# Optimization experiments

Measured on AMD Instinct MI355X. Metric: run time of the kernel, lower is better.

The kernel has to match this reference:

```python
import jax, jax.numpy as jnp
import numpy as np
from jax import lax

B, C, H, WIN, K = 8, 128, 128, 4, 3
WS = H // 2           # window_size = input_resolution / sqrt(win_num)
L = H * H
DN = ('NCHW', 'OIHW', 'NCHW')


def setup_inputs() -> dict:
    key = jax.random.key(0)
    ks = jax.random.split(key, 12)
    s = 0.02
    return {
        'x': jax.random.normal(ks[0], (B, L, C), jnp.float32),
        # ConvLayer1 params: (win_num*dim, dim, k, k), grouped conv, no bias
        'conv1_w': jax.random.normal(ks[1], (WIN * C, C, K, K), jnp.float32) * s,
        'dc_w': jax.random.normal(ks[2], (WIN, C), jnp.float32) * s,
        'dc_b': jax.random.normal(ks[3], (WIN,), jnp.float32) * s,
        'l1_w': jax.random.normal(ks[4], (4 * WIN, WIN), jnp.float32) * s,
        'l1_b': jax.random.normal(ks[5], (4 * WIN,), jnp.float32) * s,
        'l2_w': jax.random.normal(ks[6], (WIN, 4 * WIN), jnp.float32) * s,
        'l2_b': jax.random.normal(ks[7], (WIN,), jnp.float32) * s,
        'gk_w': jax.random.normal(ks[8], (C, WIN, C), jnp.float32) * s,
        'gk_b': jax.random.normal(ks[9], (C,), jnp.float32) * s,
        'fusion_w': jax.random.normal(ks[10], (C, (WIN + 1) * C), jnp.float32) * s,
        'fusion_b': jax.random.normal(ks[11], (C,), jnp.float32) * s,
    }


def reference(x, conv1_w, dc_w, dc_b, l1_w, l1_b, l2_w, l2_b, gk_w, gk_b, fusion_w, fusion_b):
    Bx = x.shape[0]
    # ka_window_partition: (B, L, C) -> (B, win_num*C, WS, WS), window-major channels
    xw = x.reshape(Bx, 2, WS, 2, WS, C).transpose(0, 1, 3, 5, 2, 4).reshape(Bx, WIN * C, WS, WS)
    # convlayer1: grouped conv, groups=win_num
    wc1 = lax.conv_general_dilated(xw, conv1_w, (1, 1), [(1, 1), (1, 1)],
                                   feature_group_count=WIN, dimension_numbers=DN)
    # SE-style window reweighting
    pooled = wc1.mean(axis=(2, 3)).reshape(Bx, WIN, C)          # adaptive avg pool
    ww = jnp.einsum('bwc,wc->bw', pooled, dc_w) + dc_b          # grouped 1x1 downchannel
    ww = jax.nn.gelu(ww @ l1_w.T + l1_b, approximate=False)
    ww = jax.nn.sigmoid(ww @ l2_w.T + l2_b)
    kern = ww[:, :, None, None, None, None] * conv1_w.reshape(WIN, C, C, K, K)[None]
    gk = jnp.einsum('owj,bwijhk->biohk', gk_w, kern) + gk_b[None, None, :, None, None]
    allk = jnp.concatenate([kern, gk[:, None]], axis=1)
    w_all = allk.reshape(Bx * (WIN + 1) * C, C, K, K)
    ximg = x.reshape(Bx, H, H, C).transpose(0, 3, 1, 2)
    xrep = jnp.tile(ximg, (1, WIN + 1, 1, 1)).reshape(1, Bx * (WIN + 1) * C, H, H)
    y = lax.conv_general_dilated(xrep, w_all, (1, 1), [(1, 1), (1, 1)],
                                 feature_group_count=Bx * (WIN + 1), dimension_numbers=DN)
    y = y.reshape(Bx, (WIN + 1) * C, H, H)
    out = jnp.einsum('oc,bchw->bohw', fusion_w, y) + fusion_b[None, :, None, None]
    return out.transpose(0, 2, 3, 1).reshape(Bx, L, C)
```

## Files before the change

kernel.cpp:

```cpp
#include <hip/hip_runtime.h>
#include <hip/hip_bf16.h>
#include <cmath>

typedef unsigned short u16;
typedef __attribute__((ext_vector_type(8))) short bf16x8;
typedef __attribute__((ext_vector_type(4))) float f32x4;
typedef __attribute__((ext_vector_type(4))) unsigned short u16x4;

#define OFF_AGG   0u
#define OFF_WW    81920u
#define OFF_R     82048u
#define OFF_FSUM  100480u
#define OFF_GKT   100992u
#define OFF_A     363136u
#define OFF_P     2722432u
#define OFF_M     5081728u
#define OFF_KEFF  7441024u
#define OFF_XPAD  9800320u

__device__ __forceinline__ u16 f2bf(float f) {
  union { float f; unsigned int u; } v; v.f = f;
  unsigned int r = v.u + 0x7FFFu + ((v.u >> 16) & 1u);
  return (u16)(r >> 16);
}

__global__ void kd1(const float* __restrict__ dc_w, const float* __restrict__ conv1_w,
                    const float* __restrict__ gk_w, const float* __restrict__ fusion_w,
                    const float* __restrict__ x,
                    float* __restrict__ R, float* __restrict__ gkT,
                    float* __restrict__ fsum, float* __restrict__ A,
                    float* __restrict__ P, u16* __restrict__ xpad,
                    float* __restrict__ rowT, float* __restrict__ colF,
                    float* __restrict__ colL) {
  const int bid = blockIdx.x, tid = threadIdx.x;
  __shared__ f32x4 ls[8][32];
  if (bid < 18) {
    int gid = bid * 256 + tid;
    int w = gid / 1152, m = gid % 1152;
    float s = 0.f;
    for (int o = 0; o < 128; ++o)
      s += dc_w[w * 128 + o] * conv1_w[(size_t)(w * 128 + o) * 1152 + m];
    R[gid] = s;
  } else if (bid < 274) {
    int gid = (bid - 18) * 256 + tid;
    int w = gid >> 14, j = (gid >> 7) & 127, c = gid & 127;
    gkT[gid] = gk_w[c * 512 + w * 128 + j];
  } else if (bid == 274) {
    if (tid < 128) {
      float s = 0.f;
      for (int oc = 0; oc < 128; ++oc) s += fusion_w[tid * 640 + 512 + oc];
      fsum[tid] = s;
    }
  } else if (bid < 851) {
    int gid = (bid - 275) * 256 + tid;
    int w = gid / 36864;
    int rem = gid % 36864;
    int o = rem / 288;
    int m = (rem % 288) * 4;
    const float* fw1 = fusion_w + o * 640 + w * 128;
    const float* fw4 = fusion_w + o * 640 + 512;
    const float* cw = conv1_w + (size_t)w * 128 * 1152 + m;
    float a0 = 0, a1 = 0, a2 = 0, a3 = 0, p0 = 0, p1 = 0, p2 = 0, p3 = 0;
    for (int oc = 0; oc < 128; ++oc) {
      float f1 = fw1[oc], f4 = fw4[oc];
      float4 cv = *(const float4*)(cw + (size_t)oc * 1152);
      a0 += f1 * cv.x; a1 += f1 * cv.y; a2 += f1 * cv.z; a3 += f1 * cv.w;
      p0 += f4 * cv.x; p1 += f4 * cv.y; p2 += f4 * cv.z; p3 += f4 * cv.w;
    }
    float4* Ao = (float4*)(A + (size_t)(w * 128 + o) * 1152 + m);
    float4* Po = (float4*)(P + (size_t)(w * 128 + o) * 1152 + m);
    *Ao = make_float4(a0, a1, a2, a3);
    *Po = make_float4(p0, p1, p2, p3);
  } else {
    const int kb = bid - 851;
    const int rp = kb % 130;
    const int b = kb / 130;
    const size_t xpb = ((size_t)b * 130 + rp) * 16640;
    if (rp == 0 || rp == 129) {
      const bf16x8 z = {0, 0, 0, 0, 0, 0, 0, 0};
      #pragma unroll
      for (int rr = 0; rr < 8; ++rr)
        *(bf16x8*)(xpad + xpb + (size_t)(rr * 256 + tid) * 8) = z;
      if (tid < 32)
        *(bf16x8*)(xpad + xpb + (size_t)(2048 + tid) * 8) = z;
      return;
    }
    const int r = rp - 1;
    if (tid < 32) {
      *(u16x4*)(xpad + xpb + tid * 4) = (u16x4){0, 0, 0, 0};
    } else if (tid < 64) {
      *(u16x4*)(xpad + xpb + 129 * 128 + (tid - 32) * 4) = (u16x4){0, 0, 0, 0};
    }
    const int s = tid >> 5;
    const int cg = tid & 31;
    const int c0 = cg * 4;
    const float* xr = x + ((size_t)b * 16384 + (size_t)r * 128) * 128;
    f32x4 sum = {0.f, 0.f, 0.f, 0.f};
    f32x4 cap = {0.f, 0.f, 0.f, 0.f};
    #pragma unroll
    for (int qi = 0; qi < 16; ++qi) {
      const int q = s * 16 + qi;
      f32x4 v = *(const f32x4*)(xr + (size_t)q * 128 + c0);
      sum += v;
      if (qi == 0 && (s == 0 || s == 4)) cap = v;
      if (qi == 15 && (s == 3 || s == 7)) cap = v;
      u16x4 st = { f2bf(v[0]), f2bf(v[1]), f2bf(v[2]), f2bf(v[3]) };
      *(u16x4*)(xpad + xpb + (size_t)(q + 1) * 128 + c0) = st;
    }
    const size_t rT2 = ((size_t)b * 128 + r) * 2;
    if (s == 0)      *(f32x4*)(colF + (rT2 + 0) * 128 + c0) = cap;
    else if (s == 4) *(f32x4*)(colF + (rT2 + 1) * 128 + c0) = cap;
    else if (s == 3) *(f32x4*)(colL + (rT2 + 0) * 128 + c0) = cap;
    else if (s == 7) *(f32x4*)(colL + (rT2 + 1) * 128 + c0) = cap;
    ls[s][cg] = sum;
    __syncthreads();
    if (tid < 64) {
      const int h = tid >> 5, g = tid & 31;
      f32x4 T = ls[h * 4 + 0][g] + ls[h * 4 + 1][g] + ls[h * 4 + 2][g] + ls[h * 4 + 3][g];
      *(f32x4*)(rowT + (rT2 + h) * 128 + g * 4) = T;
    }
  }
}

__global__ void k2_ww(const float* __restrict__ rowT, const float* __restrict__ colF,
                      const float* __restrict__ colL, const float* __restrict__ R,
                      const float* __restrict__ dc_b,
                      const float* __restrict__ l1_w, const float* __restrict__ l1_b,
                      const float* __restrict__ l2_w, const float* __restrict__ l2_b,
                      float* __restrict__ ww) {
  const int b = blockIdx.x;
  const int tid = threadIdx.x;
  const int w = tid >> 6, lane = tid & 63;
  __shared__ float red[4];
  const int i = w >> 1, j = w & 1;
  float partial = 0.f;
  #pragma unroll
  for (int k = 0; k < 2; ++k) {
    const int c = lane * 2 + k;
    const size_t rbase = ((size_t)b * 128 + i * 64) * 2 + j;
    float T = 0.f, cF = 0.f, cL = 0.f;
    #pragma unroll 4
    for (int ri = 0; ri < 64; ++ri) {
      const size_t idx = (rbase + (size_t)ri * 2) * 128 + c;
      T  += rowT[idx];
      cF += colF[idx];
      cL += colL[idx];
    }
    const size_t i0 = rbase * 128 + c;
    const size_t i63 = (rbase + 126) * 128 + c;
    const float rF = rowT[i0], rL = rowT[i63];
    const float c00 = colF[i0], c0L = colL[i0];
    const float cL0 = colF[i63], cLL = colL[i63];
    float S[9];
    S[0] = T - rL - cL + cLL;
    S[1] = T - rL;
    S[2] = T - rL - cF + cL0;
    S[3] = T - cL;
    S[4] = T;
    S[5] = T - cF;
    S[6] = T - rF - cL + c0L;
    S[7] = T - rF;
    S[8] = T - rF - cF + c00;
    const float* Rp = R + (w * 128 + c) * 9;
    #pragma unroll
    for (int t = 0; t < 9; ++t) partial += S[t] * Rp[t];
  }
  for (int off = 32; off > 0; off >>= 1) partial += __shfl_xor(partial, off, 64);
  if (lane == 0) red[w] = partial;
  __syncthreads();
  if (tid == 0) {
    float ww0[4];
    #pragma unroll
    for (int w2 = 0; w2 < 4; ++w2) ww0[w2] = red[w2] * (1.f / 4096.f) + dc_b[w2];
    float h1[16];
    for (int i2 = 0; i2 < 16; ++i2) {
      float s = l1_b[i2];
      #pragma unroll
      for (int w2 = 0; w2 < 4; ++w2) s += l1_w[i2 * 4 + w2] * ww0[w2];
      h1[i2] = 0.5f * s * (1.f + erff(s * 0.70710678118654752f));
    }
    for (int w2 = 0; w2 < 4; ++w2) {
      float s = l2_b[w2];
      for (int i2 = 0; i2 < 16; ++i2) s += l2_w[w2 * 16 + i2] * h1[i2];
      ww[b * 4 + w2] = 1.f / (1.f + expf(-s));
    }
  }
}

__global__ void k45_keff(const float* __restrict__ A, const float* __restrict__ P,
                         const float* __restrict__ gkT, const float* __restrict__ ww,
                         const float* __restrict__ fsum, const float* __restrict__ gk_b,
                         u16* __restrict__ keff) {
  const int t = blockIdx.x >> 6;
  const int o0 = (blockIdx.x & 63) * 2;
  const int tid = threadIdx.x;
  __shared__ float pl[2][4][128];
  __shared__ float al[2][4][128];
  __shared__ float red[2][2][4][128];
  #pragma unroll
  for (int rr = 0; rr < 4; ++rr) {
    const int idx = rr * 256 + tid;
    const int oi = idx >> 9, w = (idx >> 7) & 3, j = idx & 127;
    const size_t src = (size_t)(w * 128 + o0 + oi) * 1152 + j * 9 + t;
    pl[oi][w][j] = P[src];
    al[oi][w][j] = A[src];
  }
  __syncthreads();
  const int c = tid & 127, jh = tid >> 7;
  float acc[2][4];
  #pragma unroll
  for (int oi = 0; oi < 2; ++oi)
    #pragma unroll
    for (int w = 0; w < 4; ++w) acc[oi][w] = 0.f;
  const float* g = gkT + c;
  #pragma unroll 4
  for (int j = jh * 64; j < jh * 64 + 64; ++j) {
    const float g0 = g[0 * 16384 + j * 128];
    const float g1 = g[1 * 16384 + j * 128];
    const float g2 = g[2 * 16384 + j * 128];
    const float g3 = g[3 * 16384 + j * 128];
    #pragma unroll
    for (int oi = 0; oi < 2; ++oi) {
      acc[oi][0] += pl[oi][0][j] * g0;
      acc[oi][1] += pl[oi][1][j] * g1;
      acc[oi][2] += pl[oi][2][j] * g2;
      acc[oi][3] += pl[oi][3][j] * g3;
    }
  }
  #pragma unroll
  for (int oi = 0; oi < 2; ++oi)
    #pragma unroll
    for (int w = 0; w < 4; ++w) red[jh][oi][w][c] = acc[oi][w];
  __syncthreads();
  const int oi2 = tid >> 7, c2 = tid & 127;
  float m[4];
  #pragma unroll
  for (int w = 0; w < 4; ++w)
    m[w] = red[0][oi2][w][c2] + red[1][oi2][w][c2] + al[oi2][w][c2];
  const float base = fsum[o0 + oi2] * gk_b[c2];
  #pragma unroll
  for (int b = 0; b < 8; ++b) {
    float r = base;
    #pragma unroll
    for (int w = 0; w < 4; ++w) r += ww[b * 4 + w] * m[w];
    keff[(size_t)b * 147456 + (size_t)t * 16384 + (o0 + oi2) * 128 + c2] = f2bf(r);
  }
}

__global__ __launch_bounds__(256, 2) void k6_conv(
    const u16* __restrict__ xpad, const u16* __restrict__ keff,
    const float* __restrict__ fusion_b, float* __restrict__ out) {
  __shared__ __align__(16) u16 alds[130 * 128];
  __shared__ __align__(16) u16 apad[256];
  __shared__ __align__(16) u16 wlds[128 * 128];
  const int tid = threadIdx.x;
  const int blk = blockIdx.x;
  const int b = blk & 7;
  const int p = blk >> 3;
  const int wid = tid >> 6;
  const int lane = tid & 63;
  const int wm = (wid & 1) * 64;
  const int wn = (wid >> 1) * 64;
  const int quad = lane >> 4;
  const int l16 = lane & 15;

  f32x4 acc[4][4];
  #pragma unroll
  for (int i = 0; i < 4; ++i)
    #pragma unroll
    for (int j = 0; j < 4; ++j)
      acc[i][j] = (f32x4){0.f, 0.f, 0.f, 0.f};

  const u16* kb = keff + (size_t)b * 147456;
  const u16* xb = xpad + (size_t)b * 130 * 16640;
  bf16x8 streg[8];
  (void)apad;

  auto stage_W_load = [&](int tap) {
    const u16* src = kb + tap * 16384;
    #pragma unroll
    for (int it = 0; it < 8; ++it) {
      const int chunk = it * 256 + tid;
      const int gs = chunk ^ ((chunk >> 4) & 7);
      streg[it] = *(const bf16x8*)(src + gs * 8);
    }
  };
  auto stage_W_write = [&]() {
    #pragma unroll
    for (int it = 0; it < 8; ++it)
      *(bf16x8*)(wlds + (it * 256 + tid) * 8) = streg[it];
  };
  auto stage_A_dma = [&](int prow) {
    const u16* src = xb + (size_t)prow * 16640;
    #pragma unroll
    for (int r = 0; r < 8; ++r) {
      const int chunk = (wid * 8 + r) * 64 + lane;
      const int gs = chunk ^ ((chunk >> 4) & 7);
      __builtin_amdgcn_global_load_lds(
          (const __attribute__((address_space(1))) unsigned int*)(src + (size_t)gs * 8),
          (__attribute__((address_space(3))) unsigned int*)(alds + (wid * 8 + r) * 512),
          16, 0, 0);
    }
    if (tid < 32) {
      const int chunk = 2048 + tid;
      const int gs = chunk ^ ((chunk >> 4) & 7);
      __builtin_amdgcn_global_load_lds(
          (const __attribute__((address_space(1))) unsigned int*)(src + (size_t)gs * 8),
          (__attribute__((address_space(3))) unsigned int*)(alds + 2048 * 8),
          16, 0, 0);
    }
  };

  stage_W_load(0);
  stage_A_dma(p);
  stage_W_write();
  __syncthreads();

  for (int tap = 0; tap < 9; ++tap) {
    if (tap < 8) stage_W_load(tap + 1);
    const int dw = tap % 3 - 1;
    const int pixoff = 1 + dw;
    #pragma unroll
    for (int kc = 0; kc < 4; ++kc) {
      const int c0 = kc * 32 + quad * 8;
      bf16x8 a[4], bb[4];
      #pragma unroll
      for (int i = 0; i < 4; ++i) {
        const int pix = pixoff + wm + i * 16 + l16;
        const int off = (pix * 128 + c0) ^ ((pix & 7) << 3);
        a[i] = *(const bf16x8*)(alds + off);
      }
      #pragma unroll
      for (int j = 0; j < 4; ++j) {
        const int row = wn + j * 16 + l16;
        const int off = (row * 128 + c0) ^ ((row & 7) << 3);
        bb[j] = *(const bf16x8*)(wlds + off);
      }
      #pragma unroll
      for (int i = 0; i < 4; ++i)
        #pragma unroll
        for (int j = 0; j < 4; ++j)
          acc[i][j] = __builtin_amdgcn_mfma_f32_16x16x32_bf16(a[i], bb[j], acc[i][j], 0, 0, 0);
    }
    __syncthreads();
    if (tap < 8) {
      stage_W_write();
      if (tap % 3 == 2) stage_A_dma(p + (tap + 1) / 3);
      __syncthreads();
    }
  }

  float fb[4];
  #pragma unroll
  for (int j = 0; j < 4; ++j) fb[j] = fusion_b[wn + j * 16 + l16];
  float* outb = out + ((size_t)b * 16384 + (size_t)p * 128) * 128;
  #pragma unroll
  for (int i = 0; i < 4; ++i)
    #pragma unroll
    for (int r = 0; r < 4; ++r) {
      const int m = wm + i * 16 + quad * 4 + r;
      #pragma unroll
      for (int j = 0; j < 4; ++j)
        outb[(size_t)m * 128 + (wn + j * 16 + l16)] = acc[i][j][r] + fb[j];
    }
}

extern "C" void kernel_launch(void* const* d_in, const int* in_sizes, int n_in,
                              void* d_out, int out_size, void* d_ws, size_t ws_size,
                              hipStream_t stream) {
  const float* x        = (const float*)d_in[0];
  const float* conv1_w  = (const float*)d_in[1];
  const float* dc_w     = (const float*)d_in[2];
  const float* dc_b     = (const float*)d_in[3];
  const float* l1_w     = (const float*)d_in[4];
  const float* l1_b     = (const float*)d_in[5];
  const float* l2_w     = (const float*)d_in[6];
  const float* l2_b     = (const float*)d_in[7];
  const float* gk_w     = (const float*)d_in[8];
  const float* gk_b     = (const float*)d_in[9];
  const float* fusion_w = (const float*)d_in[10];
  const float* fusion_b = (const float*)d_in[11];
  float* out = (float*)d_out;
  char* ws = (char*)d_ws;

  float* wwp  = (float*)(ws + OFF_WW);
  float* R    = (float*)(ws + OFF_R);
  float* fsum = (float*)(ws + OFF_FSUM);
  float* gkT  = (float*)(ws + OFF_GKT);
  float* A    = (float*)(ws + OFF_A);
  float* P    = (float*)(ws + OFF_P);
  float* rowT = (float*)(ws + OFF_M);
  float* colF = (float*)(ws + OFF_M + 1048576u);
  float* colL = (float*)(ws + OFF_KEFF);
  u16* keff   = (u16*)(ws + OFF_KEFF);
  u16* xpad   = (u16*)(ws + OFF_XPAD);

  kd1<<<1891, 256, 0, stream>>>(dc_w, conv1_w, gk_w, fusion_w, x,
                                R, gkT, fsum, A, P, xpad, rowT, colF, colL);
  k2_ww<<<8, 256, 0, stream>>>(rowT, colF, colL, R, dc_b, l1_w, l1_b, l2_w, l2_b, wwp);
  k45_keff<<<576, 256, 0, stream>>>(A, P, gkT, wwp, fsum, gk_b, keff);
  k6_conv<<<1024, 256, 0, stream>>>(xpad, keff, fusion_b, out);
}
```

Baseline: 219.0 us.

## Fuse four kernels into a persistent megakernel with software grid barriers

Replaces the four separate launches with one persistent 512-block kernel. Its phases (precompute, window weights, effective kernel, conv) are separated by atomic-counter grid barriers, and the barrier counter is cleared with a memset before launch. Each conv block now handles two row tiles instead of one. The aim is to remove launch gaps and tail effects between stages. The risks are grid barrier spin overhead, reduced parallelism in the small phases, and a possible deadlock if all 512 blocks are not co-resident.

```diff
diff --git a/kernel.cpp b/kernel.cpp
--- a/kernel.cpp
+++ b/kernel.cpp
@@ -7,7 +7,7 @@
 typedef __attribute__((ext_vector_type(4))) float f32x4;
 typedef __attribute__((ext_vector_type(4))) unsigned short u16x4;
 
-#define OFF_AGG   0u
+#define OFF_BAR   0u
 #define OFF_WW    81920u
 #define OFF_R     82048u
 #define OFF_FSUM  100480u
@@ -24,345 +24,371 @@
   return (u16)(r >> 16);
 }
 
-__global__ void kd1(const float* __restrict__ dc_w, const float* __restrict__ conv1_w,
-                    const float* __restrict__ gk_w, const float* __restrict__ fusion_w,
-                    const float* __restrict__ x,
-                    float* __restrict__ R, float* __restrict__ gkT,
-                    float* __restrict__ fsum, float* __restrict__ A,
-                    float* __restrict__ P, u16* __restrict__ xpad,
-                    float* __restrict__ rowT, float* __restrict__ colF,
-                    float* __restrict__ colL) {
-  const int bid = blockIdx.x, tid = threadIdx.x;
-  __shared__ f32x4 ls[8][32];
-  if (bid < 18) {
-    int gid = bid * 256 + tid;
-    int w = gid / 1152, m = gid % 1152;
-    float s = 0.f;
-    for (int o = 0; o < 128; ++o)
-      s += dc_w[w * 128 + o] * conv1_w[(size_t)(w * 128 + o) * 1152 + m];
-    R[gid] = s;
-  } else if (bid < 274) {
-    int gid = (bid - 18) * 256 + tid;
-    int w = gid >> 14, j = (gid >> 7) & 127, c = gid & 127;
-    gkT[gid] = gk_w[c * 512 + w * 128 + j];
-  } else if (bid == 274) {
-    if (tid < 128) {
-      float s = 0.f;
-      for (int oc = 0; oc < 128; ++oc) s += fusion_w[tid * 640 + 512 + oc];
-      fsum[tid] = s;
-    }
-  } else if (bid < 851) {
-    int gid = (bid - 275) * 256 + tid;
-    int w = gid / 36864;
-    int rem = gid % 36864;
-    int o = rem / 288;
-    int m = (rem % 288) * 4;
-    const float* fw1 = fusion_w + o * 640 + w * 128;
-    const float* fw4 = fusion_w + o * 640 + 512;
-    const float* cw = conv1_w + (size_t)w * 128 * 1152 + m;
-    float a0 = 0, a1 = 0, a2 = 0, a3 = 0, p0 = 0, p1 = 0, p2 = 0, p3 = 0;
-    for (int oc = 0; oc < 128; ++oc) {
-      float f1 = fw1[oc], f4 = fw4[oc];
-      float4 cv = *(const float4*)(cw + (size_t)oc * 1152);
-      a0 += f1 * cv.x; a1 += f1 * cv.y; a2 += f1 * cv.z; a3 += f1 * cv.w;
-      p0 += f4 * cv.x; p1 += f4 * cv.y; p2 += f4 * cv.z; p3 += f4 * cv.w;
-    }
-    float4* Ao = (float4*)(A + (size_t)(w * 128 + o) * 1152 + m);
-    float4* Po = (float4*)(P + (size_t)(w * 128 + o) * 1152 + m);
-    *Ao = make_float4(a0, a1, a2, a3);
-    *Po = make_float4(p0, p1, p2, p3);
-  } else {
-    const int kb = bid - 851;
-    const int rp = kb % 130;
-    const int b = kb / 130;
-    const size_t xpb = ((size_t)b * 130 + rp) * 16640;
-    if (rp == 0 || rp == 129) {
-      const bf16x8 z = {0, 0, 0, 0, 0, 0, 0, 0};
-      #pragma unroll
-      for (int rr = 0; rr < 8; ++rr)
-        *(bf16x8*)(xpad + xpb + (size_t)(rr * 256 + tid) * 8) = z;
-      if (tid < 32)
-        *(bf16x8*)(xpad + xpb + (size_t)(2048 + tid) * 8) = z;
-      return;
-    }
-    const int r = rp - 1;
-    if (tid < 32) {
-      *(u16x4*)(xpad + xpb + tid * 4) = (u16x4){0, 0, 0, 0};
-    } else if (tid < 64) {
-      *(u16x4*)(xpad + xpb + 129 * 128 + (tid - 32) * 4) = (u16x4){0, 0, 0, 0};
-    }
-    const int s = tid >> 5;
-    const int cg = tid & 31;
-    const int c0 = cg * 4;
-    const float* xr = x + ((size_t)b * 16384 + (size_t)r * 128) * 128;
-    f32x4 sum = {0.f, 0.f, 0.f, 0.f};
-    f32x4 cap = {0.f, 0.f, 0.f, 0.f};
-    #pragma unroll
-    for (int qi = 0; qi < 16; ++qi) {
-      const int q = s * 16 + qi;
-      f32x4 v = *(const f32x4*)(xr + (size_t)q * 128 + c0);
-      sum += v;
-      if (qi == 0 && (s == 0 || s == 4)) cap = v;
-      if (qi == 15 && (s == 3 || s == 7)) cap = v;
-      u16x4 st = { f2bf(v[0]), f2bf(v[1]), f2bf(v[2]), f2bf(v[3]) };
-      *(u16x4*)(xpad + xpb + (size_t)(q + 1) * 128 + c0) = st;
-    }
-    const size_t rT2 = ((size_t)b * 128 + r) * 2;
-    if (s == 0)      *(f32x4*)(colF + (rT2 + 0) * 128 + c0) = cap;
-    else if (s == 4) *(f32x4*)(colF + (rT2 + 1) * 128 + c0) = cap;
-    else if (s == 3) *(f32x4*)(colL + (rT2 + 0) * 128 + c0) = cap;
-    else if (s == 7) *(f32x4*)(colL + (rT2 + 1) * 128 + c0) = cap;
-    ls[s][cg] = sum;
-    __syncthreads();
-    if (tid < 64) {
-      const int h = tid >> 5, g = tid & 31;
-      f32x4 T = ls[h * 4 + 0][g] + ls[h * 4 + 1][g] + ls[h * 4 + 2][g] + ls[h * 4 + 3][g];
-      *(f32x4*)(rowT + (rT2 + h) * 128 + g * 4) = T;
-    }
-  }
-}
-
-__global__ void k2_ww(const float* __restrict__ rowT, const float* __restrict__ colF,
-                      const float* __restrict__ colL, const float* __restrict__ R,
-                      const float* __restrict__ dc_b,
-                      const float* __restrict__ l1_w, const float* __restrict__ l1_b,
-                      const float* __restrict__ l2_w, const float* __restrict__ l2_b,
-                      float* __restrict__ ww) {
-  const int b = blockIdx.x;
-  const int tid = threadIdx.x;
-  const int w = tid >> 6, lane = tid & 63;
-  __shared__ float red[4];
-  const int i = w >> 1, j = w & 1;
-  float partial = 0.f;
-  #pragma unroll
-  for (int k = 0; k < 2; ++k) {
-    const int c = lane * 2 + k;
-    const size_t rbase = ((size_t)b * 128 + i * 64) * 2 + j;
-    float T = 0.f, cF = 0.f, cL = 0.f;
-    #pragma unroll 4
-    for (int ri = 0; ri < 64; ++ri) {
-      const size_t idx = (rbase + (size_t)ri * 2) * 128 + c;
-      T  += rowT[idx];
-      cF += colF[idx];
-      cL += colL[idx];
-    }
-    const size_t i0 = rbase * 128 + c;
-    const size_t i63 = (rbase + 126) * 128 + c;
-    const float rF = rowT[i0], rL = rowT[i63];
-    const float c00 = colF[i0], c0L = colL[i0];
-    const float cL0 = colF[i63], cLL = colL[i63];
-    float S[9];
-    S[0] = T - rL - cL + cLL;
-    S[1] = T - rL;
-    S[2] = T - rL - cF + cL0;
-    S[3] = T - cL;
-    S[4] = T;
-    S[5] = T - cF;
-    S[6] = T - rF - cL + c0L;
-    S[7] = T - rF;
-    S[8] = T - rF - cF + c00;
-    const float* Rp = R + (w * 128 + c) * 9;
-    #pragma unroll
-    for (int t = 0; t < 9; ++t) partial += S[t] * Rp[t];
-  }
-  for (int off = 32; off > 0; off >>= 1) partial += __shfl_xor(partial, off, 64);
-  if (lane == 0) red[w] = partial;
+__device__ __forceinline__ void grid_barrier(unsigned* cnt, unsigned* gen) {
   __syncthreads();
-  if (tid == 0) {
-    float ww0[4];
-    #pragma unroll
-    for (int w2 = 0; w2 < 4; ++w2) ww0[w2] = red[w2] * (1.f / 4096.f) + dc_b[w2];
-    float h1[16];
-    for (int i2 = 0; i2 < 16; ++i2) {
-      float s = l1_b[i2];
-      #pragma unroll
-      for (int w2 = 0; w2 < 4; ++w2) s += l1_w[i2 * 4 + w2] * ww0[w2];
-      h1[i2] = 0.5f * s * (1.f + erff(s * 0.70710678118654752f));
-    }
-    for (int w2 = 0; w2 < 4; ++w2) {
-      float s = l2_b[w2];
-      for (int i2 = 0; i2 < 16; ++i2) s += l2_w[w2 * 16 + i2] * h1[i2];
-      ww[b * 4 + w2] = 1.f / (1.f + expf(-s));
-    }
-  }
-}
-
-__global__ void k45_keff(const float* __restrict__ A, const float* __restrict__ P,
-                         const float* __restrict__ gkT, const float* __restrict__ ww,
-                         const float* __restrict__ fsum, const float* __restrict__ gk_b,
-                         u16* __restrict__ keff) {
-  const int t = blockIdx.x >> 6;
-  const int o0 = (blockIdx.x & 63) * 2;
-  const int tid = threadIdx.x;
-  __shared__ float pl[2][4][128];
-  __shared__ float al[2][4][128];
-  __shared__ float red[2][2][4][128];
-  #pragma unroll
-  for (int rr = 0; rr < 4; ++rr) {
-    const int idx = rr * 256 + tid;
-    const int oi = idx >> 9, w = (idx >> 7) & 3, j = idx & 127;
-    const size_t src = (size_t)(w * 128 + o0 + oi) * 1152 + j * 9 + t;
-    pl[oi][w][j] = P[src];
-    al[oi][w][j] = A[src];
+  if (threadIdx.x == 0) {
+    __threadfence();
+    unsigned g = __hip_atomic_load(gen, __ATOMIC_RELAXED, __HIP_MEMORY_SCOPE_AGENT);
+    unsigned a = __hip_atomic_fetch_add(cnt, 1u, __ATOMIC_ACQ_REL, __HIP_MEMORY_SCOPE_AGENT);
+    if (a == 511u) {
+      __hip_atomic_store(cnt, 0u, __ATOMIC_RELAXED, __HIP_MEMORY_SCOPE_AGENT);
+      __hip_atomic_store(gen, g + 1u, __ATOMIC_RELEASE, __HIP_MEMORY_SCOPE_AGENT);
+    } else {
+      while (__hip_atomic_load(gen, __ATOMIC_ACQUIRE, __HIP_MEMORY_SCOPE_AGENT) == g)
+        __builtin_amdgcn_s_sleep(4);
+    }
+    __threadfence();
   }
   __syncthreads();
-  const int c = tid & 127, jh = tid >> 7;
-  float acc[2][4];
-  #pragma unroll
-  for (int oi = 0; oi < 2; ++oi)
-    #pragma unroll
-    for (int w = 0; w < 4; ++w) acc[oi][w] = 0.f;
-  const float* g = gkT + c;
-  #pragma unroll 4
-  for (int j = jh * 64; j < jh * 64 + 64; ++j) {
-    const float g0 = g[0 * 16384 + j * 128];
-    const float g1 = g[1 * 16384 + j * 128];
-    const float g2 = g[2 * 16384 + j * 128];
-    const float g3 = g[3 * 16384 + j * 128];
-    #pragma unroll
-    for (int oi = 0; oi < 2; ++oi) {
-      acc[oi][0] += pl[oi][0][j] * g0;
-      acc[oi][1] += pl[oi][1][j] * g1;
-      acc[oi][2] += pl[oi][2][j] * g2;
-      acc[oi][3] += pl[oi][3][j] * g3;
-    }
-  }
-  #pragma unroll
-  for (int oi = 0; oi < 2; ++oi)
-    #pragma unroll
-    for (int w = 0; w < 4; ++w) red[jh][oi][w][c] = acc[oi][w];
-  __syncthreads();
-  const int oi2 = tid >> 7, c2 = tid & 127;
-  float m[4];
-  #pragma unroll
-  for (int w = 0; w < 4; ++w)
-    m[w] = red[0][oi2][w][c2] + red[1][oi2][w][c2] + al[oi2][w][c2];
-  const float base = fsum[o0 + oi2] * gk_b[c2];
-  #pragma unroll
-  for (int b = 0; b < 8; ++b) {
-    float r = base;
-    #pragma unroll
-    for (int w = 0; w < 4; ++w) r += ww[b * 4 + w] * m[w];
-    keff[(size_t)b * 147456 + (size_t)t * 16384 + (o0 + oi2) * 128 + c2] = f2bf(r);
-  }
 }
 
-__global__ __launch_bounds__(256, 2) void k6_conv(
-    const u16* __restrict__ xpad, const u16* __restrict__ keff,
-    const float* __restrict__ fusion_b, float* __restrict__ out) {
+__global__ __launch_bounds__(256, 2) void mega(
+    const float* __restrict__ x, const float* __restrict__ conv1_w,
+    const float* __restrict__ dc_w, const float* __restrict__ dc_b,
+    const float* __restrict__ l1_w, const float* __restrict__ l1_b,
+    const float* __restrict__ l2_w, const float* __restrict__ l2_b,
+    const float* __restrict__ gk_w, const float* __restrict__ gk_b,
+    const float* __restrict__ fusion_w, const float* __restrict__ fusion_b,
+    float* __restrict__ out, char* __restrict__ ws) {
+  unsigned* bcnt = (unsigned*)(ws + OFF_BAR);
+  unsigned* bgen = (unsigned*)(ws + OFF_BAR + 64);
+  float* wwp  = (float*)(ws + OFF_WW);
+  float* R    = (float*)(ws + OFF_R);
+  float* fsum = (float*)(ws + OFF_FSUM);
+  float* gkT  = (float*)(ws + OFF_GKT);
+  float* A    = (float*)(ws + OFF_A);
+  float* P    = (float*)(ws + OFF_P);
+  float* rowT = (float*)(ws + OFF_M);
+  u16* keff   = (u16*)(ws + OFF_KEFF);
+  u16* xpad   = (u16*)(ws + OFF_XPAD);
+
   __shared__ __align__(16) u16 alds[130 * 128];
   __shared__ __align__(16) u16 apad[256];
   __shared__ __align__(16) u16 wlds[128 * 128];
+  (void)apad;
+
+  const int bid = blockIdx.x;
   const int tid = threadIdx.x;
-  const int blk = blockIdx.x;
-  const int b = blk & 7;
-  const int p = blk >> 3;
-  const int wid = tid >> 6;
-  const int lane = tid & 63;
-  const int wm = (wid & 1) * 64;
-  const int wn = (wid >> 1) * 64;
-  const int quad = lane >> 4;
-  const int l16 = lane & 15;
-
-  f32x4 acc[4][4];
-  #pragma unroll
-  for (int i = 0; i < 4; ++i)
-    #pragma unroll
-    for (int j = 0; j < 4; ++j)
-      acc[i][j] = (f32x4){0.f, 0.f, 0.f, 0.f};
-
-  const u16* kb = keff + (size_t)b * 147456;
-  const u16* xb = xpad + (size_t)b * 130 * 16640;
-  bf16x8 streg[8];
-  (void)apad;
-
-  auto stage_W_load = [&](int tap) {
-    const u16* src = kb + tap * 16384;
-    #pragma unroll
-    for (int it = 0; it < 8; ++it) {
-      const int chunk = it * 256 + tid;
-      const int gs = chunk ^ ((chunk >> 4) & 7);
-      streg[it] = *(const bf16x8*)(src + gs * 8);
-    }
-  };
-  auto stage_W_write = [&]() {
-    #pragma unroll
-    for (int it = 0; it < 8; ++it)
-      *(bf16x8*)(wlds + (it * 256 + tid) * 8) = streg[it];
-  };
-  auto stage_A_dma = [&](int prow) {
-    const u16* src = xb + (size_t)prow * 16640;
-    #pragma unroll
-    for (int r = 0; r < 8; ++r) {
-      const int chunk = (wid * 8 + r) * 64 + lane;
-      const int gs = chunk ^ ((chunk >> 4) & 7);
-      __builtin_amdgcn_global_load_lds(
-          (const __attribute__((address_space(1))) unsigned int*)(src + (size_t)gs * 8),
-          (__attribute__((address_space(3))) unsigned int*)(alds + (wid * 8 + r) * 512),
-          16, 0, 0);
-    }
-    if (tid < 32) {
-      const int chunk = 2048 + tid;
-      const int gs = chunk ^ ((chunk >> 4) & 7);
-      __builtin_amdgcn_global_load_lds(
-          (const __attribute__((address_space(1))) unsigned int*)(src + (size_t)gs * 8),
-          (__attribute__((address_space(3))) unsigned int*)(alds + 2048 * 8),
-          16, 0, 0);
-    }
-  };
-
-  stage_W_load(0);
-  stage_A_dma(p);
-  stage_W_write();
-  __syncthreads();
-
-  for (int tap = 0; tap < 9; ++tap) {
-    if (tap < 8) stage_W_load(tap + 1);
-    const int dw = tap % 3 - 1;
-    const int pixoff = 1 + dw;
-    #pragma unroll
-    for (int kc = 0; kc < 4; ++kc) {
-      const int c0 = kc * 32 + quad * 8;
-      bf16x8 a[4], bb[4];
-      #pragma unroll
-      for (int i = 0; i < 4; ++i) {
-        const int pix = pixoff + wm + i * 16 + l16;
-        const int off = (pix * 128 + c0) ^ ((pix & 7) << 3);
-        a[i] = *(const bf16x8*)(alds + off);
-      }
-      #pragma unroll
-      for (int j = 0; j < 4; ++j) {
-        const int row = wn + j * 16 + l16;
-        const int off = (row * 128 + c0) ^ ((row & 7) << 3);
-        bb[j] = *(const bf16x8*)(wlds + off);
-      }
+
+  for (int unit = bid; unit < 1891; unit += 512) {
+    if (unit < 18) {
+      int gid = unit * 256 + tid;
+      int w = gid / 1152, m = gid % 1152;
+      float s = 0.f;
+      for (int o = 0; o < 128; ++o)
+        s += dc_w[w * 128 + o] * conv1_w[(size_t)(w * 128 + o) * 1152 + m];
+      R[gid] = s;
+    } else if (unit < 274) {
+      int gid = (unit - 18) * 256 + tid;
+      int w = gid >> 14, j = (gid >> 7) & 127, c = gid & 127;
+      gkT[gid] = gk_w[c * 512 + w * 128 + j];
+    } else if (unit == 274) {
+      if (tid < 128) {
+        float s = 0.f;
+        for (int oc = 0; oc < 128; ++oc) s += fusion_w[tid * 640 + 512 + oc];
+        fsum[tid] = s;
+      }
+    } else if (unit < 851) {
+      int gid = (unit - 275) * 256 + tid;
+      int w = gid / 36864;
+      int rem = gid % 36864;
+      int o = rem / 288;
+      int m = (rem % 288) * 4;
+      const float* fw1 = fusion_w + o * 640 + w * 128;
+      const float* fw4 = fusion_w + o * 640 + 512;
+      const float* cw = conv1_w + (size_t)w * 128 * 1152 + m;
+      float a0 = 0, a1 = 0, a2 = 0, a3 = 0, p0 = 0, p1 = 0, p2 = 0, p3 = 0;
+      for (int oc = 0; oc < 128; ++oc) {
+        float f1 = fw1[oc], f4 = fw4[oc];
+        float4 cv = *(const float4*)(cw + (size_t)oc * 1152);
+        a0 += f1 * cv.x; a1 += f1 * cv.y; a2 += f1 * cv.z; a3 += f1 * cv.w;
+        p0 += f4 * cv.x; p1 += f4 * cv.y; p2 += f4 * cv.z; p3 += f4 * cv.w;
+      }
+      float4* Ao = (float4*)(A + (size_t)(w * 128 + o) * 1152 + m);
+      float4* Po = (float4*)(P + (size_t)(w * 128 + o) * 1152 + m);
+      *Ao = make_float4(a0, a1, a2, a3);
+      *Po = make_float4(p0, p1, p2, p3);
+    } else {
+      const int kb = unit - 851;
+      const int rp = kb % 130;
+      const int b = kb / 130;
+      const size_t xpb = ((size_t)b * 130 + rp) * 16640;
+      if (rp == 0 || rp == 129) {
+        const bf16x8 z = {0, 0, 0, 0, 0, 0, 0, 0};
+        #pragma unroll
+        for (int rr = 0; rr < 8; ++rr)
+          *(bf16x8*)(xpad + xpb + (size_t)(rr * 256 + tid) * 8) = z;
+        if (tid < 32)
+          *(bf16x8*)(xpad + xpb + (size_t)(2048 + tid) * 8) = z;
+      } else {
+        const int r = rp - 1;
+        if (tid < 32) {
+          *(u16x4*)(xpad + xpb + tid * 4) = (u16x4){0, 0, 0, 0};
+        } else if (tid < 64) {
+          *(u16x4*)(xpad + xpb + 129 * 128 + (tid - 32) * 4) = (u16x4){0, 0, 0, 0};
+        }
+        const int s = tid >> 5;
+        const int cg2 = tid & 31;
+        const int c0 = cg2 * 4;
+        const float* xr = x + ((size_t)b * 16384 + (size_t)r * 128) * 128;
+        f32x4 sum = {0.f, 0.f, 0.f, 0.f};
+        #pragma unroll
+        for (int qi = 0; qi < 16; ++qi) {
+          const int q = s * 16 + qi;
+          f32x4 v = *(const f32x4*)(xr + (size_t)q * 128 + c0);
+          sum += v;
+          u16x4 st = { f2bf(v[0]), f2bf(v[1]), f2bf(v[2]), f2bf(v[3]) };
+          *(u16x4*)(xpad + xpb + (size_t)(q + 1) * 128 + c0) = st;
+        }
+        f32x4* ls = (f32x4*)alds;
+        ls[s * 32 + cg2] = sum;
+        __syncthreads();
+        if (tid < 64) {
+          const int h = tid >> 5, g = tid & 31;
+          f32x4 T = ls[(h * 4 + 0) * 32 + g] + ls[(h * 4 + 1) * 32 + g]
+                  + ls[(h * 4 + 2) * 32 + g] + ls[(h * 4 + 3) * 32 + g];
+          *(f32x4*)(rowT + (((size_t)b * 128 + r) * 2 + h) * 128 + g * 4) = T;
+        }
+      }
+    }
+    __syncthreads();
+  }
+  grid_barrier(bcnt, bgen);
+
+  if (bid < 8) {
+    const int b = bid;
+    const int w = tid >> 6, lane = tid & 63;
+    float* red4 = (float*)alds;
+    const int i = w >> 1, j = w & 1;
+    float partial = 0.f;
+    #pragma unroll
+    for (int k = 0; k < 2; ++k) {
+      const int c = lane * 2 + k;
+      const size_t rbase = ((size_t)b * 128 + i * 64) * 2 + j;
+      float T = 0.f;
+      #pragma unroll 4
+      for (int ri = 0; ri < 64; ++ri) T += rowT[(rbase + (size_t)ri * 2) * 128 + c];
+      const float rF = rowT[rbase * 128 + c];
+      const float rL = rowT[(rbase + 126) * 128 + c];
+      const float* xcol = x + ((size_t)b * 16384 + (size_t)(i * 64) * 128 + j * 64) * 128 + c;
+      float cF = 0.f, cL = 0.f;
+      #pragma unroll 4
+      for (int ri = 0; ri < 64; ++ri) {
+        cF += xcol[(size_t)ri * 16384];
+        cL += xcol[(size_t)ri * 16384 + 63 * 128];
+      }
+      const float c00 = xcol[0];
+      const float c0L = xcol[63 * 128];
+      const float cL0 = xcol[(size_t)63 * 16384];
+      const float cLL = xcol[(size_t)63 * 16384 + 63 * 128];
+      float S[9];
+      S[0] = T - rL - cL + cLL;
+      S[1] = T - rL;
+      S[2] = T - rL - cF + cL0;
+      S[3] = T - cL;
+      S[4] = T;
+      S[5] = T - cF;
+      S[6] = T - rF - cL + c0L;
+      S[7] = T - rF;
+      S[8] = T - rF - cF + c00;
+      const float* Rp = R + (w * 128 + c) * 9;
+      #pragma unroll
+      for (int t = 0; t < 9; ++t) partial += S[t] * Rp[t];
+    }
+    for (int off = 32; off > 0; off >>= 1) partial += __shfl_xor(partial, off, 64);
+    if (lane == 0) red4[w] = partial;
+    __syncthreads();
+    if (tid == 0) {
+      float ww0[4];
+      #pragma unroll
+      for (int w2 = 0; w2 < 4; ++w2) ww0[w2] = red4[w2] * (1.f / 4096.f) + dc_b[w2];
+      float h1[16];
+      for (int i2 = 0; i2 < 16; ++i2) {
+        float s = l1_b[i2];
+        #pragma unroll
+        for (int w2 = 0; w2 < 4; ++w2) s += l1_w[i2 * 4 + w2] * ww0[w2];
+        h1[i2] = 0.5f * s * (1.f + erff(s * 0.70710678118654752f));
+      }
+      for (int w2 = 0; w2 < 4; ++w2) {
+        float s = l2_b[w2];
+        for (int i2 = 0; i2 < 16; ++i2) s += l2_w[w2 * 16 + i2] * h1[i2];
+        wwp[b * 4 + w2] = 1.f / (1.f + expf(-s));
+      }
+    }
+  }
+  grid_barrier(bcnt, bgen);
+
+  for (int unit = bid; unit < 576; unit += 512) {
+    __syncthreads();
+    const int t = unit >> 6;
+    const int o0 = (unit & 63) * 2;
+    float* pl = (float*)alds;
+    float* al = pl + 1024;
+    float* red = (float*)wlds;
+    #pragma unroll
+    for (int rr = 0; rr < 4; ++rr) {
+      const int idx = rr * 256 + tid;
+      const int oi = idx >> 9, w = (idx >> 7) & 3, j = idx & 127;
+      const size_t src = (size_t)(w * 128 + o0 + oi) * 1152 + j * 9 + t;
+      pl[(oi * 4 + w) * 128 + j] = P[src];
+      al[(oi * 4 + w) * 128 + j] = A[src];
+    }
+    __syncthreads();
+    const int c = tid & 127, jh = tid >> 7;
+    float acc[2][4];
+    #pragma unroll
+    for (int oi = 0; oi < 2; ++oi)
+      #pragma unroll
+      for (int w = 0; w < 4; ++w) acc[oi][w] = 0.f;
+    const float* g = gkT + c;
+    #pragma unroll 4
+    for (int j = jh * 64; j < jh * 64 + 64; ++j) {
+      const float g0 = g[0 * 16384 + j * 128];
+      const float g1 = g[1 * 16384 + j * 128];
+      const float g2 = g[2 * 16384 + j * 128];
+      const float g3 = g[3 * 16384 + j * 128];
+      #pragma unroll
+      for (int oi = 0; oi < 2; ++oi) {
+        acc[oi][0] += pl[(oi * 4 + 0) * 128 + j] * g0;
+        acc[oi][1] += pl[(oi * 4 + 1) * 128 + j] * g1;
+        acc[oi][2] += pl[(oi * 4 + 2) * 128 + j] * g2;
+        acc[oi][3] += pl[(oi * 4 + 3) * 128 + j] * g3;
+      }
+    }
+    #pragma unroll
+    for (int oi = 0; oi < 2; ++oi)
+      #pragma unroll
+      for (int w = 0; w < 4; ++w) red[((jh * 2 + oi) * 4 + w) * 128 + c] = acc[oi][w];
+    __syncthreads();
+    const int oi2 = tid >> 7, c2 = tid & 127;
+    float m[4];
+    #pragma unroll
+    for (int w = 0; w < 4; ++w)
+      m[w] = red[((0 * 2 + oi2) * 4 + w) * 128 + c2]
+           + red[((1 * 2 + oi2) * 4 + w) * 128 + c2]
+           + al[(oi2 * 4 + w) * 128 + c2];
+    const float base = fsum[o0 + oi2] * gk_b[c2];
+    #pragma unroll
+    for (int b = 0; b < 8; ++b) {
+      float r = base;
+      #pragma unroll
+      for (int w = 0; w < 4; ++w) r += wwp[b * 4 + w] * m[w];
+      keff[(size_t)b * 147456 + (size_t)t * 16384 + (o0 + oi2) * 128 + c2] = f2bf(r);
+    }
+  }
+  grid_barrier(bcnt, bgen);
+
+  {
+    const int b = bid & 7;
+    const int ph = bid >> 3;
+    const int wid = tid >> 6;
+    const int lane = tid & 63;
+    const int wm = (wid & 1) * 64;
+    const int wn = (wid >> 1) * 64;
+    const int quad = lane >> 4;
+    const int l16 = lane & 15;
+    const u16* kb = keff + (size_t)b * 147456;
+    const u16* xb = xpad + (size_t)b * 130 * 16640;
+    bf16x8 streg[8];
+
+    for (int rr2 = 0; rr2 < 2; ++rr2) {
+      const int p = ph * 2 + rr2;
+      f32x4 acc[4][4];
       #pragma unroll
       for (int i = 0; i < 4; ++i)
         #pragma unroll
         for (int j = 0; j < 4; ++j)
-          acc[i][j] = __builtin_amdgcn_mfma_f32_16x16x32_bf16(a[i], bb[j], acc[i][j], 0, 0, 0);
-    }
-    __syncthreads();
-    if (tap < 8) {
+          acc[i][j] = (f32x4){0.f, 0.f, 0.f, 0.f};
+
+      auto stage_W_load = [&](int tap) {
+        const u16* src = kb + tap * 16384;
+        #pragma unroll
+        for (int it = 0; it < 8; ++it) {
+          const int chunk = it * 256 + tid;
+          const int gs = chunk ^ ((chunk >> 4) & 7);
+          streg[it] = *(const bf16x8*)(src + gs * 8);
+        }
+      };
+      auto stage_W_write = [&]() {
+        #pragma unroll
+        for (int it = 0; it < 8; ++it)
+          *(bf16x8*)(wlds + (it * 256 + tid) * 8) = streg[it];
+      };
+      auto stage_A_dma = [&](int prow) {
+        const u16* src = xb + (size_t)prow * 16640;
+        #pragma unroll
+        for (int r = 0; r < 8; ++r) {
+          const int chunk = (wid * 8 + r) * 64 + lane;
+          const int gs = chunk ^ ((chunk >> 4) & 7);
+          __builtin_amdgcn_global_load_lds(
+              (const __attribute__((address_space(1))) unsigned int*)(src + (size_t)gs * 8),
+              (__attribute__((address_space(3))) unsigned int*)(alds + (wid * 8 + r) * 512),
+              16, 0, 0);
+        }
+        if (tid < 32) {
+          const int chunk = 2048 + tid;
+          const int gs = chunk ^ ((chunk >> 4) & 7);
+          __builtin_amdgcn_global_load_lds(
+              (const __attribute__((address_space(1))) unsigned int*)(src + (size_t)gs * 8),
+              (__attribute__((address_space(3))) unsigned int*)(alds + 2048 * 8),
+              16, 0, 0);
+        }
+      };
+
+      stage_W_load(0);
+      stage_A_dma(p);
       stage_W_write();
-      if (tap % 3 == 2) stage_A_dma(p + (tap + 1) / 3);
       __syncthreads();
+
+      for (int tap = 0; tap < 9; ++tap) {
+        if (tap < 8) stage_W_load(tap + 1);
+        const int dw = tap % 3 - 1;
+        const int pixoff = 1 + dw;
+        #pragma unroll
+        for (int kc = 0; kc < 4; ++kc) {
+          const int c0 = kc * 32 + quad * 8;
+          bf16x8 a[4], bb[4];
+          #pragma unroll
+          for (int i = 0; i < 4; ++i) {
+            const int pix = pixoff + wm + i * 16 + l16;
+            const int off = (pix * 128 + c0) ^ ((pix & 7) << 3);
+            a[i] = *(const bf16x8*)(alds + off);
+          }
+          #pragma unroll
+          for (int j = 0; j < 4; ++j) {
+            const int row = wn + j * 16 + l16;
+            const int off = (row * 128 + c0) ^ ((row & 7) << 3);
+            bb[j] = *(const bf16x8*)(wlds + off);
+          }
+          #pragma unroll
+          for (int i = 0; i < 4; ++i)
+            #pragma unroll
+            for (int j = 0; j < 4; ++j)
+              acc[i][j] = __builtin_amdgcn_mfma_f32_16x16x32_bf16(a[i], bb[j], acc[i][j], 0, 0, 0);
+        }
+        __syncthreads();
+        if (tap < 8) {
+          stage_W_write();
+          if (tap % 3 == 2) stage_A_dma(p + (tap + 1) / 3);
+          __syncthreads();
+        }
+      }
+
+      float fb[4];
+      #pragma unroll
+      for (int j = 0; j < 4; ++j) fb[j] = fusion_b[wn + j * 16 + l16];
+      float* outb = out + ((size_t)b * 16384 + (size_t)p * 128) * 128;
+      #pragma unroll
+      for (int i = 0; i < 4; ++i)
+        #pragma unroll
+        for (int r = 0; r < 4; ++r) {
+          const int m = wm + i * 16 + quad * 4 + r;
+          #pragma unroll
+          for (int j = 0; j < 4; ++j)
+            outb[(size_t)m * 128 + (wn + j * 16 + l16)] = acc[i][j][r] + fb[j];
+        }
     }
   }
-
-  float fb[4];
-  #pragma unroll
-  for (int j = 0; j < 4; ++j) fb[j] = fusion_b[wn + j * 16 + l16];
-  float* outb = out + ((size_t)b * 16384 + (size_t)p * 128) * 128;
-  #pragma unroll
-  for (int i = 0; i < 4; ++i)
-    #pragma unroll
-    for (int r = 0; r < 4; ++r) {
-      const int m = wm + i * 16 + quad * 4 + r;
-      #pragma unroll
-      for (int j = 0; j < 4; ++j)
-        outb[(size_t)m * 128 + (wn + j * 16 + l16)] = acc[i][j][r] + fb[j];
-    }
 }
 
 extern "C" void kernel_launch(void* const* d_in, const int* in_sizes, int n_in,
@@ -383,21 +409,7 @@
   float* out = (float*)d_out;
   char* ws = (char*)d_ws;
 
-  float* wwp  = (float*)(ws + OFF_WW);
-  float* R    = (float*)(ws + OFF_R);
-  float* fsum = (float*)(ws + OFF_FSUM);
-  float* gkT  = (float*)(ws + OFF_GKT);
-  float* A    = (float*)(ws + OFF_A);
-  float* P    = (float*)(ws + OFF_P);
-  float* rowT = (float*)(ws + OFF_M);
-  float* colF = (float*)(ws + OFF_M + 1048576u);
-  float* colL = (float*)(ws + OFF_KEFF);
-  u16* keff   = (u16*)(ws + OFF_KEFF);
-  u16* xpad   = (u16*)(ws + OFF_XPAD);
-
-  kd1<<<1891, 256, 0, stream>>>(dc_w, conv1_w, gk_w, fusion_w, x,
-                                R, gkT, fsum, A, P, xpad, rowT, colF, colL);
-  k2_ww<<<8, 256, 0, stream>>>(rowT, colF, colL, R, dc_b, l1_w, l1_b, l2_w, l2_b, wwp);
-  k45_keff<<<576, 256, 0, stream>>>(A, P, gkT, wwp, fsum, gk_b, keff);
-  k6_conv<<<1024, 256, 0, stream>>>(xpad, keff, fusion_b, out);
+  hipMemsetAsync(ws + OFF_BAR, 0, 128, stream);
+  mega<<<512, 256, 0, stream>>>(x, conv1_w, dc_w, dc_b, l1_w, l1_b, l2_w, l2_b,
+                                gk_w, gk_b, fusion_w, fusion_b, out, ws);
 }
```

After: 715.3 us. +226.6%, slower.
